# Optimization experiments

Hardware: AMD Instinct MI355X
Metric: run time of the kernel (lower is better)

## Reference

```python
import jax, jax.numpy as jnp
import numpy as np

N = 8192
IN_F = 256
OUT_F = 128
ALPHA = 0.2
NEG = -9000000000000000.0

def setup_inputs() -> dict:
    key = jax.random.key(0)
    k1, k2, k3, k4 = jax.random.split(key, 4)
    h = jax.random.normal(k1, (N, IN_F), dtype=jnp.float32)
    adj = jax.random.randint(k2, (N, N), 0, 2, dtype=jnp.int32)
    # xavier-uniform-like params
    limW = float(np.sqrt(6.0 / (IN_F + OUT_F)))
    W = jax.random.uniform(k3, (IN_F, OUT_F), minval=-limW, maxval=limW, dtype=jnp.float32)
    lima = float(np.sqrt(6.0 / (2 * OUT_F + 1)))
    a = jax.random.uniform(k4, (2 * OUT_F, 1), minval=-lima, maxval=lima, dtype=jnp.float32)
    return {"h": h, "adj": adj, "W": W, "a": a}

def reference(h, adj, W, a):
    Wh = h @ W  # [N, F]
    # e_ij = LeakyReLU(a1.Wh_i + a2.Wh_j) -- avoids [N,N,2F] intermediate
    a1 = a[:OUT_F, 0]  # [F]
    a2 = a[OUT_F:, 0]  # [F]
    f1 = Wh @ a1  # [N]
    f2 = Wh @ a2  # [N]
    e = jax.nn.leaky_relu(f1[:, None] + f2[None, :], negative_slope=ALPHA)  # [N,N]
    att = jnp.where(adj > 0, e, jnp.float32(NEG))
    att = jax.nn.softmax(att, axis=1)
    h_prime = att @ Wh  # [N, F]
    return h_prime
```

## Files before the change

kernel.cpp:

```cpp
#include <hip/hip_runtime.h>
#include <hip/hip_bf16.h>

#define N    8192
#define INF  256
#define OUTF 128
#define ALPHA 0.2f
#define JS   16
#define NTS  (N / JS / 32)

typedef __attribute__((ext_vector_type(8))) short bf16x8;
typedef __attribute__((ext_vector_type(4))) float f32x4;

__device__ __forceinline__ unsigned short f2bf(float x) {
    union { float f; unsigned u; } v; v.f = x;
    unsigned r = v.u + 0x7fff + ((v.u >> 16) & 1);
    return (unsigned short)(r >> 16);
}

__global__ __launch_bounds__(256) void k0_pack(
        const int* __restrict__ adj, unsigned* __restrict__ bits) {
    const size_t g = (size_t)blockIdx.x * 256 + threadIdx.x;
    const int4* p = (const int4*)adj + g * 8;
    unsigned b = 0;
    #pragma unroll
    for (int u = 0; u < 8; ++u) {
        int4 v = p[u];
        b |= (v.x > 0 ? 1u : 0u) << (u * 4 + 0);
        b |= (v.y > 0 ? 1u : 0u) << (u * 4 + 1);
        b |= (v.z > 0 ? 1u : 0u) << (u * 4 + 2);
        b |= (v.w > 0 ? 1u : 0u) << (u * 4 + 3);
    }
    bits[g] = b;
}

__global__ __launch_bounds__(256) void k1_wh(
        const float* __restrict__ h, const float* __restrict__ W,
        const float* __restrict__ a,
        unsigned short* __restrict__ WhTb, float* __restrict__ f1, float* __restrict__ f2) {
    __shared__ float hs[8][INF];
    const int t  = threadIdx.x;
    const int i0 = blockIdx.x * 8;

    #pragma unroll
    for (int u = 0; u < 2; ++u) {
        int idx = u * 256 + t;
        int r   = idx >> 6;
        int kq  = idx & 63;
        *(float4*)&hs[r][kq * 4] = *(const float4*)(h + (size_t)(i0 + r) * INF + kq * 4);
    }
    __syncthreads();

    const int rg = t >> 5;
    const int ct = t & 31;
    float acc[4] = {0.f, 0.f, 0.f, 0.f};

    #pragma unroll 8
    for (int k = 0; k < INF; ++k) {
        float4 wv = *(const float4*)(W + (size_t)k * OUTF + ct * 4);
        float  hx = hs[rg][k];
        acc[0] += hx * wv.x; acc[1] += hx * wv.y;
        acc[2] += hx * wv.z; acc[3] += hx * wv.w;
    }

    const int r0 = i0 + rg;
    const int jb = r0 >> 5;
    const int jo = r0 & 31;
    #pragma unroll
    for (int cc = 0; cc < 4; ++cc)
        WhTb[(size_t)jb * 4096 + (ct * 4 + cc) * 32 + jo] = f2bf(acc[cc]);

    const float4 a1v = *(const float4*)(a + ct * 4);
    const float4 a2v = *(const float4*)(a + OUTF + ct * 4);
    float p1 = acc[0]*a1v.x + acc[1]*a1v.y + acc[2]*a1v.z + acc[3]*a1v.w;
    float p2 = acc[0]*a2v.x + acc[1]*a2v.y + acc[2]*a2v.z + acc[3]*a2v.w;
    #pragma unroll
    for (int off = 16; off > 0; off >>= 1) {
        p1 += __shfl_down(p1, off, 32);
        p2 += __shfl_down(p2, off, 32);
    }
    if (ct == 0) { f1[r0] = p1; f2[r0] = p2; }
}

__device__ __forceinline__ float pbit(float f1r, float fv, unsigned byte_,
                                      int u, float& dsum) {
    float s = f1r + fv;
    float e = fmaxf(s, ALPHA * s);
    float p = (byte_ & (1u << u)) ? __expf(e) : 0.f;
    dsum += p;
    return p;
}

#define K2SUB(WORD, JT)                                                      \
    {                                                                        \
        const int cb_ = (JT) & 1, nb_ = ((JT) + 1) & 1;                      \
        float4 sg0_, sg1_;                                                   \
        if ((JT) + 1 < NTS) {                                                \
            const char* ws_ = (const char*)WhTb + (size_t)(tile0 + (JT) + 1) * 8192; \
            sg0_ = *(const float4*)(ws_ + t * 16);                           \
            sg1_ = *(const float4*)(ws_ + 4096 + t * 16);                    \
        }                                                                    \
        float4 F0_ = *(const float4*)&f2s[(JT) * 32 + quad * 8];             \
        float4 F1_ = *(const float4*)&f2s[(JT) * 32 + quad * 8 + 4];         \
        unsigned byte_ = ((WORD) >> (quad << 3)) & 0xffu;                    \
        float p0_ = pbit(f1r, F0_.x, byte_, 0, dsum);                        \
        float p1_ = pbit(f1r, F0_.y, byte_, 1, dsum);                        \
        float p2_ = pbit(f1r, F0_.z, byte_, 2, dsum);                        \
        float p3_ = pbit(f1r, F0_.w, byte_, 3, dsum);                        \
        float p4_ = pbit(f1r, F1_.x, byte_, 4, dsum);                        \
        float p5_ = pbit(f1r, F1_.y, byte_, 5, dsum);                        \
        float p6_ = pbit(f1r, F1_.z, byte_, 6, dsum);                        \
        float p7_ = pbit(f1r, F1_.w, byte_, 7, dsum);                        \
        union { __hip_bfloat162 hh[4]; bf16x8 v; } pk_;                      \
        pk_.hh[0] = __float22bfloat162_rn(make_float2(p0_, p1_));            \
        pk_.hh[1] = __float22bfloat162_rn(make_float2(p2_, p3_));            \
        pk_.hh[2] = __float22bfloat162_rn(make_float2(p4_, p5_));            \
        pk_.hh[3] = __float22bfloat162_rn(make_float2(p6_, p7_));            \
        bf16x8 afrag = pk_.v;                                                \
        const char* bb_ = (const char*)&bsm[cb_][0] + laneb2;                \
        bf16x8 b0_ = *(const bf16x8*)(bb_);                                  \
        bf16x8 b1_ = *(const bf16x8*)(bb_ + 1024);                           \
        bf16x8 b2_ = *(const bf16x8*)(bb_ + 2048);                           \
        bf16x8 b3_ = *(const bf16x8*)(bb_ + 3072);                           \
        bf16x8 b4_ = *(const bf16x8*)(bb_ + 4096);                           \
        bf16x8 b5_ = *(const bf16x8*)(bb_ + 5120);                           \
        bf16x8 b6_ = *(const bf16x8*)(bb_ + 6144);                           \
        bf16x8 b7_ = *(const bf16x8*)(bb_ + 7168);                           \
        acc0 = __builtin_amdgcn_mfma_f32_16x16x32_bf16(afrag, b0_, acc0, 0, 0, 0); \
        acc1 = __builtin_amdgcn_mfma_f32_16x16x32_bf16(afrag, b1_, acc1, 0, 0, 0); \
        acc2 = __builtin_amdgcn_mfma_f32_16x16x32_bf16(afrag, b2_, acc2, 0, 0, 0); \
        acc3 = __builtin_amdgcn_mfma_f32_16x16x32_bf16(afrag, b3_, acc3, 0, 0, 0); \
        acc4 = __builtin_amdgcn_mfma_f32_16x16x32_bf16(afrag, b4_, acc4, 0, 0, 0); \
        acc5 = __builtin_amdgcn_mfma_f32_16x16x32_bf16(afrag, b5_, acc5, 0, 0, 0); \
        acc6 = __builtin_amdgcn_mfma_f32_16x16x32_bf16(afrag, b6_, acc6, 0, 0, 0); \
        acc7 = __builtin_amdgcn_mfma_f32_16x16x32_bf16(afrag, b7_, acc7, 0, 0, 0); \
        if ((JT) + 1 < NTS) {                                                \
            char* bd_ = (char*)&bsm[nb_][0];                                 \
            *(float4*)(bd_ + t * 16)        = sg0_;                          \
            *(float4*)(bd_ + 4096 + t * 16) = sg1_;                          \
        }                                                                    \
        __syncthreads();                                                     \
    }

__global__ __launch_bounds__(256, 5) void k2_attn(
        const unsigned* __restrict__ bits, const unsigned short* __restrict__ WhTb,
        const float* __restrict__ f1, const float* __restrict__ f2,
        float* __restrict__ num, float* __restrict__ den) {
    __shared__ unsigned short bsm[2][4096];
    __shared__ float f2s[512];

    const int t    = threadIdx.x;
    const int wv   = t >> 6;
    const int ln   = t & 63;
    const int m16  = ln & 15;
    const int quad = ln >> 4;
    const int i0   = blockIdx.x * 64;
    const int s    = blockIdx.y;
    const int row  = i0 + wv * 16 + m16;
    const int tile0 = s * NTS;
    const int j0    = s * (N / JS);
    const int laneb2 = (m16 * 32 + quad * 8) * 2;

    if (t < 128) *(float4*)&f2s[t * 4] = *(const float4*)(f2 + j0 + t * 4);
    {
        const char* ws0 = (const char*)WhTb + (size_t)tile0 * 8192;
        float4 s0 = *(const float4*)(ws0 + t * 16);
        float4 s1 = *(const float4*)(ws0 + 4096 + t * 16);
        char* bd = (char*)&bsm[0][0];
        *(float4*)(bd + t * 16)        = s0;
        *(float4*)(bd + 4096 + t * 16) = s1;
    }

    const float f1r = f1[row];
    const uint4* brow = (const uint4*)((const char*)bits + (size_t)row * 1024 + (size_t)tile0 * 4);
    uint4 bw0 = brow[0], bw1 = brow[1], bw2 = brow[2], bw3 = brow[3];

    f32x4 acc0 = {0.f,0.f,0.f,0.f}, acc1 = {0.f,0.f,0.f,0.f};
    f32x4 acc2 = {0.f,0.f,0.f,0.f}, acc3 = {0.f,0.f,0.f,0.f};
    f32x4 acc4 = {0.f,0.f,0.f,0.f}, acc5 = {0.f,0.f,0.f,0.f};
    f32x4 acc6 = {0.f,0.f,0.f,0.f}, acc7 = {0.f,0.f,0.f,0.f};
    float dsum = 0.f;

    __syncthreads();

    K2SUB(bw0.x,  0) K2SUB(bw0.y,  1) K2SUB(bw0.z,  2) K2SUB(bw0.w,  3)
    K2SUB(bw1.x,  4) K2SUB(bw1.y,  5) K2SUB(bw1.z,  6) K2SUB(bw1.w,  7)
    K2SUB(bw2.x,  8) K2SUB(bw2.y,  9) K2SUB(bw2.z, 10) K2SUB(bw2.w, 11)
    K2SUB(bw3.x, 12) K2SUB(bw3.y, 13) K2SUB(bw3.z, 14) K2SUB(bw3.w, 15)

    dsum += __shfl_xor(dsum, 16);
    dsum += __shfl_xor(dsum, 32);
    if (quad == 0) den[(size_t)s * N + row] = dsum;

    float* np = num + (size_t)s * N * OUTF;
    #pragma unroll
    for (int r = 0; r < 4; ++r) {
        const size_t orow = (size_t)(i0 + wv * 16 + quad * 4 + r) * OUTF;
        np[orow + 0 * 16 + m16] = acc0[r];
        np[orow + 1 * 16 + m16] = acc1[r];
        np[orow + 2 * 16 + m16] = acc2[r];
        np[orow + 3 * 16 + m16] = acc3[r];
        np[orow + 4 * 16 + m16] = acc4[r];
        np[orow + 5 * 16 + m16] = acc5[r];
        np[orow + 6 * 16 + m16] = acc6[r];
        np[orow + 7 * 16 + m16] = acc7[r];
    }
}

__global__ __launch_bounds__(256) void k3_combine(
        const float* __restrict__ num, const float* __restrict__ den,
        float* __restrict__ out) {
    const int idx = blockIdx.x * 256 + threadIdx.x;
    const int row = idx >> 5;
    const int c4  = (idx & 31) * 4;
    float4 ns = {0.f,0.f,0.f,0.f};
    float  ds = 0.f;
    #pragma unroll
    for (int s = 0; s < JS; ++s) {
        float4 nv = *(const float4*)(num + ((size_t)s * N + row) * OUTF + c4);
        ns.x += nv.x; ns.y += nv.y; ns.z += nv.z; ns.w += nv.w;
        ds += den[(size_t)s * N + row];
    }
    const float inv = 1.0f / ds;
    float4 o = {ns.x * inv, ns.y * inv, ns.z * inv, ns.w * inv};
    *(float4*)(out + (size_t)row * OUTF + c4) = o;
}

extern "C" void kernel_launch(void* const* d_in, const int* in_sizes, int n_in,
                              void* d_out, int out_size, void* d_ws, size_t ws_size,
                              hipStream_t stream) {
    const float* h   = (const float*)d_in[0];
    const int*   adj = (const int*)  d_in[1];
    const float* W   = (const float*)d_in[2];
    const float* a   = (const float*)d_in[3];
    float* out = (float*)d_out;

    unsigned short* WhTb = (unsigned short*)d_ws;
    float*    f1   = (float*)(WhTb + (size_t)N * OUTF);
    float*    f2   = f1 + N;
    float*    den  = f2 + N;
    unsigned* bits = (unsigned*)(den + (size_t)JS * N);
    float*    num  = (float*)(bits + (size_t)N * (N / 32));

    k1_wh     <<<N / 8, 256, 0, stream>>>(h, W, a, WhTb, f1, f2);
    k0_pack   <<<(N / 32) * (N / 256), 256, 0, stream>>>(adj, bits);
    k2_attn   <<<dim3(N / 64, JS), 256, 0, stream>>>(bits, WhTb, f1, f2, num, den);
    k3_combine<<<(N * OUTF / 4) / 256, 256, 0, stream>>>(num, den, out);
}
```

Baseline: 452.8 us.

## Fuse prep kernels, use direct global-to-LDS loads, halve j-splits in attention

The Wh and adjacency-pack kernels are merged into one launch, with blocks split by index, to remove a launch and let the two phases overlap. The attention kernel now stages Wh tiles with global_load_lds instead of a register round trip. It loops over more tiles per block because JS drops from 16 to 8, and it prefetches adjacency words one group ahead instead of loading them all up front. This trades fewer partial sums and less combine traffic for longer per-block loops and lower occupancy (launch bounds 5 to 4).

```diff
diff --git a/kernel.cpp b/kernel.cpp
--- a/kernel.cpp
+++ b/kernel.cpp
@@ -5,7 +5,7 @@
 #define INF  256
 #define OUTF 128
 #define ALPHA 0.2f
-#define JS   16
+#define JS   8
 #define NTS  (N / JS / 32)
 
 typedef __attribute__((ext_vector_type(8))) short bf16x8;
@@ -17,30 +17,37 @@
     return (unsigned short)(r >> 16);
 }
 
-__global__ __launch_bounds__(256) void k0_pack(
-        const int* __restrict__ adj, unsigned* __restrict__ bits) {
-    const size_t g = (size_t)blockIdx.x * 256 + threadIdx.x;
-    const int4* p = (const int4*)adj + g * 8;
-    unsigned b = 0;
-    #pragma unroll
-    for (int u = 0; u < 8; ++u) {
-        int4 v = p[u];
-        b |= (v.x > 0 ? 1u : 0u) << (u * 4 + 0);
-        b |= (v.y > 0 ? 1u : 0u) << (u * 4 + 1);
-        b |= (v.z > 0 ? 1u : 0u) << (u * 4 + 2);
-        b |= (v.w > 0 ? 1u : 0u) << (u * 4 + 3);
-    }
-    bits[g] = b;
-}
-
-__global__ __launch_bounds__(256) void k1_wh(
+__device__ __forceinline__ void gll16(const void* g, void* l) {
+    __builtin_amdgcn_global_load_lds(
+        (const __attribute__((address_space(1))) unsigned*)g,
+        (__attribute__((address_space(3))) unsigned*)l, 16, 0, 0);
+}
+
+__global__ __launch_bounds__(256) void k01_prep(
+        const int* __restrict__ adj, unsigned* __restrict__ bits,
         const float* __restrict__ h, const float* __restrict__ W,
         const float* __restrict__ a,
         unsigned short* __restrict__ WhTb, float* __restrict__ f1, float* __restrict__ f2) {
     __shared__ float hs[8][INF];
-    const int t  = threadIdx.x;
+    const int t = threadIdx.x;
+
+    if (blockIdx.x >= 1024) {
+        const size_t g = (size_t)(blockIdx.x - 1024) * 256 + t;
+        const int4* p = (const int4*)adj + g * 8;
+        unsigned b = 0;
+        #pragma unroll
+        for (int u = 0; u < 8; ++u) {
+            int4 v = p[u];
+            b |= (v.x > 0 ? 1u : 0u) << (u * 4 + 0);
+            b |= (v.y > 0 ? 1u : 0u) << (u * 4 + 1);
+            b |= (v.z > 0 ? 1u : 0u) << (u * 4 + 2);
+            b |= (v.w > 0 ? 1u : 0u) << (u * 4 + 3);
+        }
+        bits[g] = b;
+        return;
+    }
+
     const int i0 = blockIdx.x * 8;
-
     #pragma unroll
     for (int u = 0; u < 2; ++u) {
         int idx = u * 256 + t;
@@ -90,14 +97,13 @@
     return p;
 }
 
-#define K2SUB(WORD, JT)                                                      \
+#define K2SUB(WORD, PH, JT)                                                  \
     {                                                                        \
-        const int cb_ = (JT) & 1, nb_ = ((JT) + 1) & 1;                      \
-        float4 sg0_, sg1_;                                                   \
         if ((JT) + 1 < NTS) {                                                \
             const char* ws_ = (const char*)WhTb + (size_t)(tile0 + (JT) + 1) * 8192; \
-            sg0_ = *(const float4*)(ws_ + t * 16);                           \
-            sg1_ = *(const float4*)(ws_ + 4096 + t * 16);                    \
+            char* bd_ = (char*)&bsm[(PH) ^ 1][0];                            \
+            gll16(ws_ + t * 16,        bd_ + wv * 1024 + 0);                 \
+            gll16(ws_ + 4096 + t * 16, bd_ + 4096 + wv * 1024 + 0);          \
         }                                                                    \
         float4 F0_ = *(const float4*)&f2s[(JT) * 32 + quad * 8];             \
         float4 F1_ = *(const float4*)&f2s[(JT) * 32 + quad * 8 + 4];         \
@@ -116,7 +122,7 @@
         pk_.hh[2] = __float22bfloat162_rn(make_float2(p4_, p5_));            \
         pk_.hh[3] = __float22bfloat162_rn(make_float2(p6_, p7_));            \
         bf16x8 afrag = pk_.v;                                                \
-        const char* bb_ = (const char*)&bsm[cb_][0] + laneb2;                \
+        const char* bb_ = (const char*)&bsm[PH][0] + laneb2;                 \
         bf16x8 b0_ = *(const bf16x8*)(bb_);                                  \
         bf16x8 b1_ = *(const bf16x8*)(bb_ + 1024);                           \
         bf16x8 b2_ = *(const bf16x8*)(bb_ + 2048);                           \
@@ -133,20 +139,15 @@
         acc5 = __builtin_amdgcn_mfma_f32_16x16x32_bf16(afrag, b5_, acc5, 0, 0, 0); \
         acc6 = __builtin_amdgcn_mfma_f32_16x16x32_bf16(afrag, b6_, acc6, 0, 0, 0); \
         acc7 = __builtin_amdgcn_mfma_f32_16x16x32_bf16(afrag, b7_, acc7, 0, 0, 0); \
-        if ((JT) + 1 < NTS) {                                                \
-            char* bd_ = (char*)&bsm[nb_][0];                                 \
-            *(float4*)(bd_ + t * 16)        = sg0_;                          \
-            *(float4*)(bd_ + 4096 + t * 16) = sg1_;                          \
-        }                                                                    \
         __syncthreads();                                                     \
     }
 
-__global__ __launch_bounds__(256, 5) void k2_attn(
+__global__ __launch_bounds__(256, 4) void k2_attn(
         const unsigned* __restrict__ bits, const unsigned short* __restrict__ WhTb,
         const float* __restrict__ f1, const float* __restrict__ f2,
         float* __restrict__ num, float* __restrict__ den) {
     __shared__ unsigned short bsm[2][4096];
-    __shared__ float f2s[512];
+    __shared__ float f2s[1024];
 
     const int t    = threadIdx.x;
     const int wv   = t >> 6;
@@ -160,19 +161,16 @@
     const int j0    = s * (N / JS);
     const int laneb2 = (m16 * 32 + quad * 8) * 2;
 
-    if (t < 128) *(float4*)&f2s[t * 4] = *(const float4*)(f2 + j0 + t * 4);
+    *(float4*)&f2s[t * 4] = *(const float4*)(f2 + j0 + t * 4);
     {
         const char* ws0 = (const char*)WhTb + (size_t)tile0 * 8192;
-        float4 s0 = *(const float4*)(ws0 + t * 16);
-        float4 s1 = *(const float4*)(ws0 + 4096 + t * 16);
         char* bd = (char*)&bsm[0][0];
-        *(float4*)(bd + t * 16)        = s0;
-        *(float4*)(bd + 4096 + t * 16) = s1;
+        gll16(ws0 + t * 16,        bd + wv * 1024);
+        gll16(ws0 + 4096 + t * 16, bd + 4096 + wv * 1024);
     }
 
     const float f1r = f1[row];
-    const uint4* brow = (const uint4*)((const char*)bits + (size_t)row * 1024 + (size_t)tile0 * 4);
-    uint4 bw0 = brow[0], bw1 = brow[1], bw2 = brow[2], bw3 = brow[3];
+    const uint4* brow = (const uint4*)(bits + (size_t)row * 256 + tile0);
 
     f32x4 acc0 = {0.f,0.f,0.f,0.f}, acc1 = {0.f,0.f,0.f,0.f};
     f32x4 acc2 = {0.f,0.f,0.f,0.f}, acc3 = {0.f,0.f,0.f,0.f};
@@ -180,12 +178,18 @@
     f32x4 acc6 = {0.f,0.f,0.f,0.f}, acc7 = {0.f,0.f,0.f,0.f};
     float dsum = 0.f;
 
+    uint4 bwc = brow[0];
     __syncthreads();
 
-    K2SUB(bw0.x,  0) K2SUB(bw0.y,  1) K2SUB(bw0.z,  2) K2SUB(bw0.w,  3)
-    K2SUB(bw1.x,  4) K2SUB(bw1.y,  5) K2SUB(bw1.z,  6) K2SUB(bw1.w,  7)
-    K2SUB(bw2.x,  8) K2SUB(bw2.y,  9) K2SUB(bw2.z, 10) K2SUB(bw2.w, 11)
-    K2SUB(bw3.x, 12) K2SUB(bw3.y, 13) K2SUB(bw3.z, 14) K2SUB(bw3.w, 15)
+    for (int g = 0; g < NTS / 4; ++g) {
+        uint4 bwn = brow[(g + 1 < NTS / 4) ? g + 1 : g];
+        const int jtb = g * 4;
+        K2SUB(bwc.x, 0, jtb + 0)
+        K2SUB(bwc.y, 1, jtb + 1)
+        K2SUB(bwc.z, 0, jtb + 2)
+        K2SUB(bwc.w, 1, jtb + 3)
+        bwc = bwn;
+    }
 
     dsum += __shfl_xor(dsum, 16);
     dsum += __shfl_xor(dsum, 32);
@@ -241,8 +245,7 @@
     unsigned* bits = (unsigned*)(den + (size_t)JS * N);
     float*    num  = (float*)(bits + (size_t)N * (N / 32));
 
-    k1_wh     <<<N / 8, 256, 0, stream>>>(h, W, a, WhTb, f1, f2);
-    k0_pack   <<<(N / 32) * (N / 256), 256, 0, stream>>>(adj, bits);
+    k01_prep  <<<1024 + (N / 32) * (N / 256), 256, 0, stream>>>(adj, bits, h, W, a, WhTb, f1, f2);
     k2_attn   <<<dim3(N / 64, JS), 256, 0, stream>>>(bits, WhTb, f1, f2, num, den);
     k3_combine<<<(N * OUTF / 4) / 256, 256, 0, stream>>>(num, den, out);
 }
```

Result: faster. 431.4 us (-4.7%).
